# Optimization experiments

Hardware: AMD Instinct MI355X
Metric: run time of the kernel (lower is better)

The kernel has to match this reference:

```python
import jax, jax.numpy as jnp
import numpy as np
from itertools import product

D = 96  # input grid resolution; after subdivision it is 2*D = 192
N_VOX = 20000
C_IN = 64
C_OUT = 64

OFFSETS = jnp.array(list(product([-1, 0, 1], repeat=3)), dtype=jnp.int32)   # [27,3] conv neighborhood
CHILD = jnp.array(list(product([0, 1], repeat=3)), dtype=jnp.int32)        # [8,3] subdivision children


def _lin(coords, d):
    # linearize (z,y,x)-style coords into a flat index for the dense lookup grid
    return (coords[:, 0] * d + coords[:, 1]) * d + coords[:, 2]


def _submanifold_conv3d(coords, feats, W, b, d):
    """Submanifold sparse 3x3x3 conv: output only at active sites.
    coords: [N,3] int32, feats: [N,Cin], W: [27,Cin,Cout], b: [Cout]."""
    n = coords.shape[0]
    grid = jnp.full((d * d * d,), -1, dtype=jnp.int32).at[_lin(coords, d)].set(
        jnp.arange(n, dtype=jnp.int32))
    out = jnp.broadcast_to(b, (n, b.shape[0])).astype(feats.dtype)
    for k in range(27):  # fixed small kernel loop (unrolled under jit)
        nb = coords + OFFSETS[k]
        inb = jnp.all((nb >= 0) & (nb < d), axis=1)
        idx = grid[_lin(jnp.clip(nb, 0, d - 1), d)]
        mask = (inb & (idx >= 0)).astype(feats.dtype)
        f = feats[jnp.maximum(idx, 0)] * mask[:, None]  # gather active neighbors
        out = out + f @ W[k]
    return out


def setup_inputs() -> dict:
    rng = np.random.default_rng(0)
    lin = rng.choice(D ** 3, size=N_VOX, replace=False)  # unique active voxels
    coords = np.stack([lin // (D * D), (lin // D) % D, lin % D], axis=1).astype(np.int32)
    key = jax.random.key(0)
    k1, k2, k3, k4, k5 = jax.random.split(key, 5)
    scale = 1.0 / np.sqrt(27.0 * C_IN)
    return {
        "coords": jnp.asarray(coords),
        "feats": jax.random.normal(k1, (N_VOX, C_IN), jnp.float32),
        "W1": jax.random.normal(k2, (27, C_IN, C_OUT), jnp.float32) * scale,
        "b1": jax.random.normal(k3, (C_OUT,), jnp.float32) * 0.01,
        "W2": jax.random.normal(k4, (27, C_OUT, C_OUT), jnp.float32) * scale,
        "b2": jax.random.normal(k5, (C_OUT,), jnp.float32) * 0.01,
    }


def reference(coords, feats, W1, b1, W2, b2):
    # act_layers: SparseConv3d + SiLU
    h = jax.nn.silu(_submanifold_conv3d(coords, feats, W1, b1, D))
    n = coords.shape[0]
    coords2 = ((coords * 2)[:, None, :] + CHILD[None, :, :]).reshape(8 * n, 3)
    h2 = jnp.repeat(h, 8, axis=0)  # matches (N,8,C)->(8N,C) child order
    # out_layers: SparseConv3d + SiLU at doubled resolution
    return jax.nn.silu(_submanifold_conv3d(coords2, h2, W2, b2, 2 * D))
```

## Files before the change

kernel.cpp:

```cpp
#include <hip/hip_runtime.h>

#define D1 96
#define GRID_VOX (D1 * D1 * D1)
#define CAP1 32
#define CAP2S 8

typedef __attribute__((ext_vector_type(8))) short short8_t;
typedef __attribute__((ext_vector_type(4))) float f32x4;

__device__ __forceinline__ unsigned short bf16rne(float x) {
    unsigned u = __float_as_uint(x);
    return (unsigned short)((u + 0x7FFF + ((u >> 16) & 1)) >> 16);
}
__device__ __forceinline__ void split2(float v, unsigned short& hi,
                                       unsigned short& lo) {
    hi = bf16rne(v);
    float hf = __uint_as_float((unsigned)hi << 16);
    lo = bf16rne(v - hf);
}

__global__ void scatter_grid_kernel(const int* __restrict__ coords,
                                    unsigned short* __restrict__ grid, int n) {
    int i = blockIdx.x * blockDim.x + threadIdx.x;
    if (i < n)
        grid[(coords[3 * i] * D1 + coords[3 * i + 1]) * D1 + coords[3 * i + 2]] =
            (unsigned short)(i + 1);
}

__global__ void prep_weights_kernel(const float* __restrict__ W1,
                                    const float* __restrict__ W2,
                                    unsigned short* __restrict__ Wpk1h,
                                    unsigned short* __restrict__ Wpk1l,
                                    unsigned short* __restrict__ Wpk2h,
                                    unsigned short* __restrict__ Wpk2l,
                                    float* __restrict__ W2e) {
    int t = blockIdx.x * blockDim.x + threadIdx.x;
    if (t < 512) {
        int fid = t >> 6, l = t & 63;
        int kb = fid >> 2, c = fid & 3;
#pragma unroll
        for (int e = 0; e < 8; ++e) {
            int ci = kb * 32 + ((l >> 4) << 3) + e;
            int co = c * 16 + (l & 15);
            unsigned short hi, lo;
            split2(W1[13 * 4096 + ci * 64 + co], hi, lo);
            Wpk1h[(size_t)t * 8 + e] = hi;
            Wpk1l[(size_t)t * 8 + e] = lo;
        }
    } else if (t < 512 + 4096) {
        int u = t - 512;
        int fid = u >> 6, l = u & 63;
        int s = fid >> 3, kb = (fid >> 2) & 1, c = fid & 3;
        int s0 = (s >> 2) & 1, s1 = (s >> 1) & 1, s2 = s & 1;
#pragma unroll
        for (int e = 0; e < 8; ++e) {
            int ci = kb * 32 + ((l >> 4) << 3) + e;
            int co = c * 16 + (l & 15);
            float sum = 0.f;
            for (int o0 = -s0; o0 <= 1 - s0; ++o0)
                for (int o1 = -s1; o1 <= 1 - s1; ++o1)
                    for (int o2 = -s2; o2 <= 1 - s2; ++o2) {
                        int k = (o0 + 1) * 9 + (o1 + 1) * 3 + (o2 + 1);
                        sum += W2[k * 4096 + ci * 64 + co];
                    }
            unsigned short hi, lo;
            split2(sum, hi, lo);
            Wpk2h[(size_t)u * 8 + e] = hi;
            Wpk2l[(size_t)u * 8 + e] = lo;
        }
    } else {
        int r = t - 4608;
        if (r >= 64 * 4096) return;
        int sd = r >> 12, e = r & 4095;
        int s = sd >> 3, d = sd & 7;
        int sa[3] = { (s >> 2) & 1, (s >> 1) & 1, s & 1 };
        int da[3] = { (d >> 2) & 1, (d >> 1) & 1, d & 1 };
        int lo_[3], hi_[3];
        for (int a = 0; a < 3; ++a) {
            int p = sa[a] - 1 + da[a];
            int l = 2 * p - sa[a];     if (l < -1) l = -1;
            int h = 2 * p + 1 - sa[a]; if (h > 1) h = 1;
            lo_[a] = l; hi_[a] = h;
        }
        float sum = 0.f;
        for (int o0 = lo_[0]; o0 <= hi_[0]; ++o0)
            for (int o1 = lo_[1]; o1 <= hi_[1]; ++o1)
                for (int o2 = lo_[2]; o2 <= hi_[2]; ++o2) {
                    int k = (o0 + 1) * 9 + (o1 + 1) * 3 + (o2 + 1);
                    sum += W2[k * 4096 + e];
                }
        W2e[(size_t)sd * 4096 + e] = sum;
    }
}

__global__ void build_pairs_kernel(const int* __restrict__ coords,
                                   const unsigned short* __restrict__ grid,
                                   int* __restrict__ c1, int* __restrict__ p1,
                                   int* __restrict__ c2s, int* __restrict__ p2s,
                                   int n) {
    int i = blockIdx.x * blockDim.x + threadIdx.x;
    if (i >= n) return;
    int c0 = coords[3 * i], cc1 = coords[3 * i + 1], cc2 = coords[3 * i + 2];

    int jv[27];
#pragma unroll
    for (int k = 0; k < 27; ++k) {
        int o0 = k / 9 - 1, o1 = (k / 3) % 3 - 1, o2 = k % 3 - 1;
        int x0 = c0 + o0, x1 = cc1 + o1, x2 = cc2 + o2;
        bool inb = (unsigned)x0 < D1 && (unsigned)x1 < D1 && (unsigned)x2 < D1;
        jv[k] = inb ? (int)grid[(x0 * D1 + x1) * D1 + x2] - 1 : -1;
    }

    int n1 = 0;
    int n2[8] = {0, 0, 0, 0, 0, 0, 0, 0};
#pragma unroll
    for (int k = 0; k < 27; ++k) {
        if (k == 13) continue;
        int j = jv[k];
        if (j < 0) continue;
        int o0 = k / 9 - 1, o1 = (k / 3) % 3 - 1, o2 = k % 3 - 1;
        p1[(size_t)i * CAP1 + n1] = j | (k << 17);
        ++n1;
#pragma unroll
        for (int s = 0; s < 8; ++s) {
            int d0 = o0 + 1 - ((s >> 2) & 1);
            int d1 = o1 + 1 - ((s >> 1) & 1);
            int d2 = o2 + 1 - (s & 1);
            if (((d0 | d1 | d2) & ~1) == 0) {
                int d = (d0 << 2) | (d1 << 1) | d2;
                p2s[((size_t)i * 8 + s) * CAP2S + n2[s]] = j | (d << 17);
                ++n2[s];
            }
        }
    }
    c1[i] = n1;
#pragma unroll
    for (int s = 0; s < 8; ++s) c2s[i * 8 + s] = n2[s];
}

__device__ __forceinline__ void dense_mfma(const float* __restrict__ src,
                                           int arow,
                                           const short8_t* __restrict__ Bh,
                                           const short8_t* __restrict__ Bl,
                                           const float* __restrict__ bias,
                                           float* __restrict__ oT, int w,
                                           int lane) {
    const float* ap = src + (size_t)arow * 64 + ((lane >> 4) << 3);
    f32x4 a0 = *(const f32x4*)(ap);
    f32x4 a1 = *(const f32x4*)(ap + 4);
    f32x4 a2 = *(const f32x4*)(ap + 32);
    f32x4 a3 = *(const f32x4*)(ap + 36);

    short8_t ah0, al0, ah1, al1;
#pragma unroll
    for (int e = 0; e < 4; ++e) {
        unsigned short hh, ll;
        split2(a0[e], hh, ll); ah0[e] = (short)hh; al0[e] = (short)ll;
        split2(a1[e], hh, ll); ah0[4 + e] = (short)hh; al0[4 + e] = (short)ll;
        split2(a2[e], hh, ll); ah1[e] = (short)hh; al1[e] = (short)ll;
        split2(a3[e], hh, ll); ah1[4 + e] = (short)hh; al1[4 + e] = (short)ll;
    }

#pragma unroll 1
    for (int c = 0; c < 4; ++c) {
        short8_t bh0 = Bh[c * 64 + lane];
        short8_t bl0 = Bl[c * 64 + lane];
        short8_t bh1 = Bh[(4 + c) * 64 + lane];
        short8_t bl1 = Bl[(4 + c) * 64 + lane];
        f32x4 acc = {0.f, 0.f, 0.f, 0.f};
        acc = __builtin_amdgcn_mfma_f32_16x16x32_bf16(ah0, bh0, acc, 0, 0, 0);
        acc = __builtin_amdgcn_mfma_f32_16x16x32_bf16(al0, bh0, acc, 0, 0, 0);
        acc = __builtin_amdgcn_mfma_f32_16x16x32_bf16(ah0, bl0, acc, 0, 0, 0);
        acc = __builtin_amdgcn_mfma_f32_16x16x32_bf16(ah1, bh1, acc, 0, 0, 0);
        acc = __builtin_amdgcn_mfma_f32_16x16x32_bf16(al1, bh1, acc, 0, 0, 0);
        acc = __builtin_amdgcn_mfma_f32_16x16x32_bf16(ah1, bl1, acc, 0, 0, 0);
        int col = c * 16 + (lane & 15);
        float bb = bias[col];
#pragma unroll
        for (int r = 0; r < 4; ++r) {
            int row = w * 16 + ((lane >> 4) << 2) + r;
            oT[row * 64 + col] = acc[r] + bb;
        }
    }
}

__device__ __forceinline__ void fixup_pair(const float* __restrict__ fj,
                                           const float* __restrict__ wk,
                                           float* __restrict__ oT, int l,
                                           int lane) {
    float a0 = 0.f, a1 = 0.f, a2 = 0.f, a3 = 0.f;
#pragma unroll
    for (int c4 = 0; c4 < 16; ++c4) {
        f32x4 fv = *(const f32x4*)(fj + c4 * 4);
        a0 += fv[0] * wk[(c4 * 4 + 0) * 64 + lane];
        a1 += fv[1] * wk[(c4 * 4 + 1) * 64 + lane];
        a2 += fv[2] * wk[(c4 * 4 + 2) * 64 + lane];
        a3 += fv[3] * wk[(c4 * 4 + 3) * 64 + lane];
    }
    atomicAdd(&oT[l * 64 + lane], (a0 + a1) + (a2 + a3));
}

__global__ __launch_bounds__(256) void conv1_fused_kernel(
    const float* __restrict__ feats, const float* __restrict__ W1,
    const unsigned short* __restrict__ Wpk1h,
    const unsigned short* __restrict__ Wpk1l, const float* __restrict__ b1,
    const int* __restrict__ c1, const int* __restrict__ p1,
    float* __restrict__ h, int n) {
    __shared__ __align__(16) float oT[4096];
    __shared__ int pl[1 + 64 * 26];
    int base = blockIdx.x * 64;
    int t = threadIdx.x, w = t >> 6, lane = t & 63;

    if (t == 0) pl[0] = 0;
    __syncthreads();
    if (t < 64) {
        int row = base + t;
        int cnt = (row < n) ? c1[row] : 0;
        if (cnt > 0) {
            int off = atomicAdd(pl, cnt);
            for (int e = 0; e < cnt; ++e)
                pl[1 + off + e] = p1[(size_t)row * CAP1 + e] | (t << 23);
        }
    }

    int arow = base + w * 16 + (lane & 15);
    if (arow >= n) arow = n - 1;
    dense_mfma(feats, arow, (const short8_t*)Wpk1h, (const short8_t*)Wpk1l,
               b1, oT, w, lane);
    __syncthreads();

    int np = pl[0];
    for (int p = w; p < np; p += 4) {
        int se = pl[1 + p];
        se = __builtin_amdgcn_readfirstlane(se);
        int j = se & 0x1FFFF, k = (se >> 17) & 31, l = (se >> 23) & 63;
        fixup_pair(feats + (size_t)j * 64, W1 + (size_t)k * 4096, oT, l, lane);
    }
    __syncthreads();

    {
        int r = t >> 2, q0 = (t & 3) * 16;
        if (base + r < n) {
#pragma unroll
            for (int jj = 0; jj < 4; ++jj) {
                f32x4 v = *(f32x4*)&oT[r * 64 + q0 + jj * 4];
#pragma unroll
                for (int u = 0; u < 4; ++u) v[u] = v[u] / (1.f + __expf(-v[u]));
                *(f32x4*)&h[(size_t)(base + r) * 64 + q0 + jj * 4] = v;
            }
        }
    }
}

__global__ __launch_bounds__(256) void conv2_fused_kernel(
    const float* __restrict__ h, const unsigned short* __restrict__ Wpk2h,
    const unsigned short* __restrict__ Wpk2l, const float* __restrict__ W2e,
    const float* __restrict__ b2, const int* __restrict__ c2s,
    const int* __restrict__ p2s, float* __restrict__ out, int n) {
    __shared__ __align__(16) float oT[4096];
    __shared__ int pl[1 + 64 * 7];
    int base = blockIdx.x * 64, s = blockIdx.y;
    int t = threadIdx.x, w = t >> 6, lane = t & 63;

    if (t == 0) pl[0] = 0;
    __syncthreads();
    if (t < 64) {
        int row = base + t;
        int cnt = (row < n) ? c2s[(size_t)row * 8 + s] : 0;
        if (cnt > 0) {
            int off = atomicAdd(pl, cnt);
            for (int e = 0; e < cnt; ++e)
                pl[1 + off + e] = p2s[((size_t)row * 8 + s) * CAP2S + e] | (t << 23);
        }
    }

    int arow = base + w * 16 + (lane & 15);
    if (arow >= n) arow = n - 1;
    dense_mfma(h, arow, (const short8_t*)Wpk2h + (size_t)s * 8 * 64,
               (const short8_t*)Wpk2l + (size_t)s * 8 * 64, b2, oT, w, lane);
    __syncthreads();

    int np = pl[0];
    for (int p = w; p < np; p += 4) {
        int se = pl[1 + p];
        se = __builtin_amdgcn_readfirstlane(se);
        int j = se & 0x1FFFF, d = (se >> 17) & 31, l = (se >> 23) & 63;
        fixup_pair(h + (size_t)j * 64, W2e + (size_t)(s * 8 + d) * 4096, oT, l,
                   lane);
    }
    __syncthreads();

    {
        int r = t >> 2, q0 = (t & 3) * 16;
        if (base + r < n) {
#pragma unroll
            for (int jj = 0; jj < 4; ++jj) {
                f32x4 v = *(f32x4*)&oT[r * 64 + q0 + jj * 4];
#pragma unroll
                for (int u = 0; u < 4; ++u) v[u] = v[u] / (1.f + __expf(-v[u]));
                *(f32x4*)&out[((size_t)(base + r) * 8 + s) * 64 + q0 + jj * 4] = v;
            }
        }
    }
}

extern "C" void kernel_launch(void* const* d_in, const int* in_sizes, int n_in,
                              void* d_out, int out_size, void* d_ws,
                              size_t ws_size, hipStream_t stream) {
    const int* coords = (const int*)d_in[0];
    const float* feats = (const float*)d_in[1];
    const float* W1 = (const float*)d_in[2];
    const float* b1 = (const float*)d_in[3];
    const float* W2 = (const float*)d_in[4];
    const float* b2 = (const float*)d_in[5];
    float* out = (float*)d_out;

    int n = in_sizes[0] / 3;

    char* ws = (char*)d_ws;
    size_t off = 0;
    auto alloc = [&](size_t bytes) {
        size_t o = off;
        off = (off + bytes + 255) & ~(size_t)255;
        return o;
    };
    unsigned short* grid1 = (unsigned short*)(ws + alloc((size_t)GRID_VOX * 2));
    float* h      = (float*)(ws + alloc((size_t)n * 64 * 4));
    float* W2e    = (float*)(ws + alloc(64 * 4096 * 4));
    unsigned short* Wpk1h = (unsigned short*)(ws + alloc(512 * 8 * 2));
    unsigned short* Wpk1l = (unsigned short*)(ws + alloc(512 * 8 * 2));
    unsigned short* Wpk2h = (unsigned short*)(ws + alloc(4096 * 8 * 2));
    unsigned short* Wpk2l = (unsigned short*)(ws + alloc(4096 * 8 * 2));
    int*   c1     = (int*)(ws + alloc((size_t)n * 9 * 4));
    int*   c2s    = c1 + n;
    int*   p1     = (int*)(ws + alloc((size_t)n * CAP1 * 4));
    int*   p2s    = (int*)(ws + alloc((size_t)n * 8 * CAP2S * 4));

    hipMemsetAsync(grid1, 0, (size_t)GRID_VOX * 2, stream);

    scatter_grid_kernel<<<(n + 255) / 256, 256, 0, stream>>>(coords, grid1, n);
    prep_weights_kernel<<<(4608 + 64 * 4096 + 255) / 256, 256, 0, stream>>>(
        W1, W2, Wpk1h, Wpk1l, Wpk2h, Wpk2l, W2e);
    build_pairs_kernel<<<(n + 255) / 256, 256, 0, stream>>>(
        coords, grid1, c1, p1, c2s, p2s, n);

    int nblk = (n + 63) / 64;
    conv1_fused_kernel<<<nblk, 256, 0, stream>>>(feats, W1, Wpk1h, Wpk1l, b1,
                                                 c1, p1, h, n);
    conv2_fused_kernel<<<dim3(nblk, 8), 256, 0, stream>>>(
        h, Wpk2h, Wpk2l, W2e, b2, c2s, p2s, out, n);
}
```

Measured before the change: 90.29 us.

## Fuse grid memset into weight prep and reuse split A across four subdivision children

The hipMemsetAsync of the lookup grid is folded into a combined setup kernel that zeroes the grid with int4 stores in extra blocks, which removes one launch. Conv2 now launches 2 y-blocks instead of 8, and each block loops over 4 children, loading and bf16-splitting its A rows once and reusing them. This cuts redundant global loads and split arithmetic. In exchange the conv2 grid has a quarter as many blocks and each block runs serially with more barriers, which may lower occupancy and latency hiding.

```diff
diff --git a/kernel.cpp b/kernel.cpp
--- a/kernel.cpp
+++ b/kernel.cpp
@@ -19,22 +19,20 @@
     lo = bf16rne(v - hf);
 }
 
-__global__ void scatter_grid_kernel(const int* __restrict__ coords,
-                                    unsigned short* __restrict__ grid, int n) {
-    int i = blockIdx.x * blockDim.x + threadIdx.x;
-    if (i < n)
-        grid[(coords[3 * i] * D1 + coords[3 * i + 1]) * D1 + coords[3 * i + 2]] =
-            (unsigned short)(i + 1);
-}
-
-__global__ void prep_weights_kernel(const float* __restrict__ W1,
-                                    const float* __restrict__ W2,
-                                    unsigned short* __restrict__ Wpk1h,
-                                    unsigned short* __restrict__ Wpk1l,
-                                    unsigned short* __restrict__ Wpk2h,
-                                    unsigned short* __restrict__ Wpk2l,
-                                    float* __restrict__ W2e) {
-    int t = blockIdx.x * blockDim.x + threadIdx.x;
+__global__ void setup_kernel(const float* __restrict__ W1,
+                             const float* __restrict__ W2,
+                             int4* __restrict__ grid16,
+                             unsigned short* __restrict__ Wpk1h,
+                             unsigned short* __restrict__ Wpk1l,
+                             unsigned short* __restrict__ Wpk2h,
+                             unsigned short* __restrict__ Wpk2l,
+                             float* __restrict__ W2e) {
+    int b = blockIdx.x;
+    if (b < 432) {
+        grid16[b * 256 + threadIdx.x] = make_int4(0, 0, 0, 0);
+        return;
+    }
+    int t = (b - 432) * 256 + threadIdx.x;
     if (t < 512) {
         int fid = t >> 6, l = t & 63;
         int kb = fid >> 2, c = fid & 3;
@@ -93,6 +91,14 @@
     }
 }
 
+__global__ void scatter_grid_kernel(const int* __restrict__ coords,
+                                    unsigned short* __restrict__ grid, int n) {
+    int i = blockIdx.x * blockDim.x + threadIdx.x;
+    if (i < n)
+        grid[(coords[3 * i] * D1 + coords[3 * i + 1]) * D1 + coords[3 * i + 2]] =
+            (unsigned short)(i + 1);
+}
+
 __global__ void build_pairs_kernel(const int* __restrict__ coords,
                                    const unsigned short* __restrict__ grid,
                                    int* __restrict__ c1, int* __restrict__ p1,
@@ -138,20 +144,15 @@
     for (int s = 0; s < 8; ++s) c2s[i * 8 + s] = n2[s];
 }
 
-__device__ __forceinline__ void dense_mfma(const float* __restrict__ src,
-                                           int arow,
-                                           const short8_t* __restrict__ Bh,
-                                           const short8_t* __restrict__ Bl,
-                                           const float* __restrict__ bias,
-                                           float* __restrict__ oT, int w,
-                                           int lane) {
+__device__ __forceinline__ void load_split_A(const float* __restrict__ src,
+                                             int arow, int lane, short8_t& ah0,
+                                             short8_t& al0, short8_t& ah1,
+                                             short8_t& al1) {
     const float* ap = src + (size_t)arow * 64 + ((lane >> 4) << 3);
     f32x4 a0 = *(const f32x4*)(ap);
     f32x4 a1 = *(const f32x4*)(ap + 4);
     f32x4 a2 = *(const f32x4*)(ap + 32);
     f32x4 a3 = *(const f32x4*)(ap + 36);
-
-    short8_t ah0, al0, ah1, al1;
 #pragma unroll
     for (int e = 0; e < 4; ++e) {
         unsigned short hh, ll;
@@ -160,7 +161,15 @@
         split2(a2[e], hh, ll); ah1[e] = (short)hh; al1[e] = (short)ll;
         split2(a3[e], hh, ll); ah1[4 + e] = (short)hh; al1[4 + e] = (short)ll;
     }
-
+}
+
+__device__ __forceinline__ void dense_mfma(const short8_t ah0, const short8_t al0,
+                                           const short8_t ah1, const short8_t al1,
+                                           const short8_t* __restrict__ Bh,
+                                           const short8_t* __restrict__ Bl,
+                                           const float* __restrict__ bias,
+                                           float* __restrict__ oT, int w,
+                                           int lane) {
 #pragma unroll 1
     for (int c = 0; c < 4; ++c) {
         short8_t bh0 = Bh[c * 64 + lane];
@@ -225,8 +234,10 @@
 
     int arow = base + w * 16 + (lane & 15);
     if (arow >= n) arow = n - 1;
-    dense_mfma(feats, arow, (const short8_t*)Wpk1h, (const short8_t*)Wpk1l,
-               b1, oT, w, lane);
+    short8_t ah0, al0, ah1, al1;
+    load_split_A(feats, arow, lane, ah0, al0, ah1, al1);
+    dense_mfma(ah0, al0, ah1, al1, (const short8_t*)Wpk1h,
+               (const short8_t*)Wpk1l, b1, oT, w, lane);
     __syncthreads();
 
     int np = pl[0];
@@ -259,48 +270,61 @@
     const int* __restrict__ p2s, float* __restrict__ out, int n) {
     __shared__ __align__(16) float oT[4096];
     __shared__ int pl[1 + 64 * 7];
-    int base = blockIdx.x * 64, s = blockIdx.y;
+    int base = blockIdx.x * 64;
     int t = threadIdx.x, w = t >> 6, lane = t & 63;
-
-    if (t == 0) pl[0] = 0;
-    __syncthreads();
-    if (t < 64) {
-        int row = base + t;
-        int cnt = (row < n) ? c2s[(size_t)row * 8 + s] : 0;
-        if (cnt > 0) {
-            int off = atomicAdd(pl, cnt);
-            for (int e = 0; e < cnt; ++e)
-                pl[1 + off + e] = p2s[((size_t)row * 8 + s) * CAP2S + e] | (t << 23);
-        }
-    }
 
     int arow = base + w * 16 + (lane & 15);
     if (arow >= n) arow = n - 1;
-    dense_mfma(h, arow, (const short8_t*)Wpk2h + (size_t)s * 8 * 64,
-               (const short8_t*)Wpk2l + (size_t)s * 8 * 64, b2, oT, w, lane);
-    __syncthreads();
-
-    int np = pl[0];
-    for (int p = w; p < np; p += 4) {
-        int se = pl[1 + p];
-        se = __builtin_amdgcn_readfirstlane(se);
-        int j = se & 0x1FFFF, d = (se >> 17) & 31, l = (se >> 23) & 63;
-        fixup_pair(h + (size_t)j * 64, W2e + (size_t)(s * 8 + d) * 4096, oT, l,
+    short8_t ah0, al0, ah1, al1;
+    load_split_A(h, arow, lane, ah0, al0, ah1, al1);
+
+#pragma unroll 1
+    for (int sl = 0; sl < 4; ++sl) {
+        int s = blockIdx.y * 4 + sl;
+
+        if (t == 0) pl[0] = 0;
+        __syncthreads();
+        if (t < 64) {
+            int row = base + t;
+            int cnt = (row < n) ? c2s[(size_t)row * 8 + s] : 0;
+            if (cnt > 0) {
+                int off = atomicAdd(pl, cnt);
+                for (int e = 0; e < cnt; ++e)
+                    pl[1 + off + e] =
+                        p2s[((size_t)row * 8 + s) * CAP2S + e] | (t << 23);
+            }
+        }
+        dense_mfma(ah0, al0, ah1, al1,
+                   (const short8_t*)Wpk2h + (size_t)s * 8 * 64,
+                   (const short8_t*)Wpk2l + (size_t)s * 8 * 64, b2, oT, w,
                    lane);
-    }
-    __syncthreads();
-
-    {
-        int r = t >> 2, q0 = (t & 3) * 16;
-        if (base + r < n) {
-#pragma unroll
-            for (int jj = 0; jj < 4; ++jj) {
-                f32x4 v = *(f32x4*)&oT[r * 64 + q0 + jj * 4];
-#pragma unroll
-                for (int u = 0; u < 4; ++u) v[u] = v[u] / (1.f + __expf(-v[u]));
-                *(f32x4*)&out[((size_t)(base + r) * 8 + s) * 64 + q0 + jj * 4] = v;
+        __syncthreads();
+
+        int np = pl[0];
+        for (int p = w; p < np; p += 4) {
+            int se = pl[1 + p];
+            se = __builtin_amdgcn_readfirstlane(se);
+            int j = se & 0x1FFFF, d = (se >> 17) & 31, l = (se >> 23) & 63;
+            fixup_pair(h + (size_t)j * 64, W2e + (size_t)(s * 8 + d) * 4096,
+                       oT, l, lane);
+        }
+        __syncthreads();
+
+        {
+            int r = t >> 2, q0 = (t & 3) * 16;
+            if (base + r < n) {
+#pragma unroll
+                for (int jj = 0; jj < 4; ++jj) {
+                    f32x4 v = *(f32x4*)&oT[r * 64 + q0 + jj * 4];
+#pragma unroll
+                    for (int u = 0; u < 4; ++u)
+                        v[u] = v[u] / (1.f + __expf(-v[u]));
+                    *(f32x4*)&out[((size_t)(base + r) * 8 + s) * 64 + q0 +
+                                  jj * 4] = v;
+                }
             }
         }
+        __syncthreads();
     }
 }
 
@@ -336,17 +360,15 @@
     int*   p1     = (int*)(ws + alloc((size_t)n * CAP1 * 4));
     int*   p2s    = (int*)(ws + alloc((size_t)n * 8 * CAP2S * 4));
 
-    hipMemsetAsync(grid1, 0, (size_t)GRID_VOX * 2, stream);
-
+    setup_kernel<<<432 + 1042, 256, 0, stream>>>(
+        W1, W2, (int4*)grid1, Wpk1h, Wpk1l, Wpk2h, Wpk2l, W2e);
     scatter_grid_kernel<<<(n + 255) / 256, 256, 0, stream>>>(coords, grid1, n);
-    prep_weights_kernel<<<(4608 + 64 * 4096 + 255) / 256, 256, 0, stream>>>(
-        W1, W2, Wpk1h, Wpk1l, Wpk2h, Wpk2l, W2e);
     build_pairs_kernel<<<(n + 255) / 256, 256, 0, stream>>>(
         coords, grid1, c1, p1, c2s, p2s, n);
 
     int nblk = (n + 63) / 64;
     conv1_fused_kernel<<<nblk, 256, 0, stream>>>(feats, W1, Wpk1h, Wpk1l, b1,
                                                  c1, p1, h, n);
-    conv2_fused_kernel<<<dim3(nblk, 8), 256, 0, stream>>>(
+    conv2_fused_kernel<<<dim3(nblk, 2), 256, 0, stream>>>(
         h, Wpk2h, Wpk2l, W2e, b2, c2s, p2s, out, n);
 }
```

Measured after the change: 92.78 us. +2.8%, slower.
